# Performance work log

Measured on AMD Instinct MI355X. Metric: run time of the kernel, lower is better.

Reference implementation:

```python
import jax, jax.numpy as jnp
import numpy as np

EMB_DIM = 128
NUM_CLS = 128
H = W = 512
K = 131072


def setup_inputs() -> dict:
    key = jax.random.key(0)
    k1, k2, k3, k4 = jax.random.split(key, 4)
    gc_features = jax.random.normal(k1, (1, EMB_DIM, H, W), dtype=jnp.float32)
    cls_id_map = jax.random.randint(k2, (1, K), 0, H * W, dtype=jnp.int64)
    # nn.Linear(emb_dim, num_cls) params, kaiming-uniform-ish scale
    lim = 1.0 / np.sqrt(EMB_DIM)
    W_cls = jax.random.uniform(k3, (NUM_CLS, EMB_DIM), dtype=jnp.float32, minval=-lim, maxval=lim)
    b_cls = jax.random.uniform(k4, (NUM_CLS,), dtype=jnp.float32, minval=-lim, maxval=lim)
    return {"gc_features": gc_features, "cls_id_map": cls_id_map, "W_cls": W_cls, "b_cls": b_cls}


def reference(gc_features, cls_id_map, W_cls, b_cls):
    B, C, h, w = gc_features.shape
    # _tranpose_and_gather_feat: [B,C,H,W] -> [B,HW,C], gather rows by inds
    feat = gc_features.reshape(B, C, h * w).transpose(0, 2, 1)      # [B, HW, C]
    feat = jnp.take_along_axis(feat, cls_id_map[:, :, None], axis=1)  # [B, K, C]
    feat = feat[0]                                                   # squeeze(0) -> [K, C]
    pred = feat @ W_cls.T + b_cls                                    # [K, num_cls]
    return jax.nn.softmax(pred, axis=1)
```

## Files before the change

### kernel.cpp

```cpp
#include <hip/hip_runtime.h>
#include <hip/hip_bf16.h>
#include <hip/hip_fp16.h>

#define HW      262144
#define NCH     128
#define NCLS    128
#define KROWS   131072
#define NTILE   4096
#define CAP     192

typedef short  bf16x8 __attribute__((ext_vector_type(8)));
typedef float  f32x4  __attribute__((ext_vector_type(4)));

__device__ inline ushort f2bf(float f) {
    union { float f; unsigned u; } v; v.f = f;
    unsigned u = v.u;
    unsigned r = (u + 0x7FFFu + ((u >> 16) & 1u)) >> 16;
    return (ushort)r;
}

__global__ __launch_bounds__(256) void prep(const float* __restrict__ Wc,
                                            ushort* __restrict__ Wf,
                                            int4* __restrict__ cnt4) {
    if (blockIdx.x < 64) {
        int e    = blockIdx.x * 256 + threadIdx.x;
        int j    = e & 7;
        int slot = e >> 3;
        int lane = slot & 63;
        int kk   = (slot >> 6) & 3;
        int nt   = slot >> 8;
        int n = (nt << 4) + (lane & 15);
        int k = (kk << 5) + ((lane >> 4) << 3) + j;
        Wf[e] = f2bf(Wc[n * NCH + k]);
    } else {
        cnt4[(blockIdx.x - 64) * 256 + threadIdx.x] = make_int4(0, 0, 0, 0);
    }
}

__global__ __launch_bounds__(256) void csr_fill(const int* __restrict__ idx,
                                                int* __restrict__ cnt,
                                                int* __restrict__ pairs) {
    int k = blockIdx.x * 256 + threadIdx.x;
    int p = idx[k];
    int tile = p >> 6;
    int pos = atomicAdd(&cnt[tile], 1);
    if (pos < CAP) pairs[tile * CAP + pos] = (k << 6) | (p & 63);
}

__global__ __launch_bounds__(256) void gemm_scatter(const float* __restrict__ gc,
                                                    const ushort* __restrict__ Wf,
                                                    const float* __restrict__ bias,
                                                    const int* __restrict__ cnt,
                                                    const int* __restrict__ pairs,
                                                    float* __restrict__ out) {
    __shared__ ushort Wl[NCLS * NCH];
    __shared__ ushort AO[64 * NCH];

    const int t    = threadIdx.x;
    const int lane = t & 63;
    const int wv   = t >> 6;
    const int l15  = lane & 15;
    const int quad = lane >> 4;
    const int m0   = blockIdx.x << 6;

    float4 va[8];
    #pragma unroll
    for (int i = 0; i < 4; ++i) {
        int q  = (i << 8) + t;
        int cp = q >> 4, mq = q & 15;
        int c0 = cp << 1, m = mq << 2;
        va[2 * i]     = *(const float4*)&gc[(size_t)c0 * HW + m0 + m];
        va[2 * i + 1] = *(const float4*)&gc[(size_t)(c0 + 1) * HW + m0 + m];
    }

    #pragma unroll
    for (int i = 0; i < 8; ++i) {
        const ushort* g = Wf + (i << 11) + (t << 3);
        ushort*       l = Wl + (i << 11) + (t << 3);
        __builtin_amdgcn_global_load_lds(
            (const __attribute__((address_space(1))) unsigned*)g,
            (__attribute__((address_space(3))) unsigned*)l, 16, 0, 0);
    }

    float bcol[8];
    #pragma unroll
    for (int nt = 0; nt < 8; ++nt) bcol[nt] = bias[(nt << 4) + l15];

    #pragma unroll
    for (int i = 0; i < 4; ++i) {
        int q  = (i << 8) + t;
        int cp = q >> 4, mq = q & 15;
        int c0 = cp << 1, m = mq << 2;
        int kk = c0 >> 5, kc2 = (c0 >> 3) & 3, j = c0 & 7;
        const float* a0 = (const float*)&va[2 * i];
        const float* a1 = (const float*)&va[2 * i + 1];
        #pragma unroll
        for (int d = 0; d < 4; ++d) {
            int row  = m + d;
            int slot = ((((row >> 4) << 2) + kk) << 6) + (row & 15) + (kc2 << 4);
            slot ^= (row >> 2) & 7;
            __hip_bfloat162 pk = __float22bfloat162_rn(make_float2(a0[d], a1[d]));
            *(ushort2*)&AO[(slot << 3) + j] = *(ushort2*)&pk;
        }
    }
    __syncthreads();

    f32x4 acc[8];
    #pragma unroll
    for (int i = 0; i < 8; ++i) acc[i] = (f32x4){0.f, 0.f, 0.f, 0.f};

    #pragma unroll
    for (int kk = 0; kk < 4; ++kk) {
        int aslot = ((((wv << 2) + kk) << 6) + lane) ^ ((((wv << 4) + l15) >> 2) & 7);
        bf16x8 a = *(const bf16x8*)&AO[aslot << 3];
        #pragma unroll
        for (int nt = 0; nt < 8; ++nt) {
            bf16x8 b = *(const bf16x8*)&Wl[((((nt << 2) + kk) << 6) + lane) << 3];
            acc[nt] = __builtin_amdgcn_mfma_f32_16x16x32_bf16(a, b, acc[nt], 0, 0, 0);
        }
    }

    float inv[4];
    #pragma unroll
    for (int rr = 0; rr < 4; ++rr) {
        float s = 0.f;
        #pragma unroll
        for (int nt = 0; nt < 8; ++nt) {
            acc[nt][rr] = __expf(acc[nt][rr] + bcol[nt]);
            s += acc[nt][rr];
        }
        s += __shfl_xor(s, 1, 64);
        s += __shfl_xor(s, 2, 64);
        s += __shfl_xor(s, 4, 64);
        s += __shfl_xor(s, 8, 64);
        inv[rr] = 1.0f / s;
    }

    const int g = ((quad & 1) << 2) | (quad & 2);
    #pragma unroll
    for (int nt = 0; nt < 8; ++nt) {
        int cl = ((nt << 1) + (l15 >> 3)) ^ g;
        #pragma unroll
        for (int rr = 0; rr < 4; ++rr) {
            int row = (wv << 4) + (quad << 2) + rr;
            AO[(row << 7) + (cl << 3) + (l15 & 7)] =
                __half_as_ushort(__float2half_rn(acc[nt][rr] * inv[rr]));
        }
    }
    __syncthreads();

    const int nb = min(cnt[blockIdx.x], CAP);
    const int* pb = pairs + blockIdx.x * CAP;
    #pragma unroll 2
    for (int e = wv; e < nb; e += 4) {
        int pk  = pb[e];
        int row = pk & 63;
        int k   = pk >> 6;
        int qd  = (row >> 2) & 3;
        int gq  = ((qd & 1) << 2) | (qd & 2);
        int cl  = (lane >> 2) ^ gq;
        __half2 h = *(const __half2*)&AO[(row << 7) + (cl << 3) + ((lane << 1) & 7)];
        float2 f = __half22float2(h);
        *(float2*)&out[((size_t)k << 7) + (lane << 1)] = f;
    }
}

extern "C" void kernel_launch(void* const* d_in, const int* in_sizes, int n_in,
                              void* d_out, int out_size, void* d_ws, size_t ws_size,
                              hipStream_t stream) {
    const float* gc   = (const float*)d_in[0];
    const int*   idx  = (const int*)d_in[1];
    const float* Wc   = (const float*)d_in[2];
    const float* bias = (const float*)d_in[3];
    float* out = (float*)d_out;

    char* ws = (char*)d_ws;
    int*    cnt   = (int*)(ws);
    int*    pairs = (int*)(ws + 0x10000);
    ushort* Wf    = (ushort*)(ws + 0x400000);

    prep        <<<dim3(68),       dim3(256), 0, stream>>>(Wc, Wf, (int4*)cnt);
    csr_fill    <<<dim3(KROWS/256),dim3(256), 0, stream>>>(idx, cnt, pairs);
    gemm_scatter<<<dim3(NTILE),    dim3(256), 0, stream>>>(gc, Wf, bias, cnt, pairs, out);
}
```

Before: 236.6 us.

## Fuse prep, CSR fill and GEMM into one persistent cooperative kernel

Replaces the three kernel launches with a single persistent cooperative kernel. Each block converts W to bf16 directly into LDS, zeroes the counters, and issues its first tile's feature loads. It then passes a grid sync, builds the CSR bucket lists, syncs again, and loops over tiles while prefetching the next tile's features into registers. This removes two launch gaps and overlaps the first feature loads with the bucketing phase, at the cost of two grid-wide barriers, redundant per-block W conversion, and lower occupancy from persistent scheduling with extra registers.

```diff
diff --git a/kernel.cpp b/kernel.cpp
--- a/kernel.cpp
+++ b/kernel.cpp
@@ -1,6 +1,9 @@
 #include <hip/hip_runtime.h>
 #include <hip/hip_bf16.h>
 #include <hip/hip_fp16.h>
+#include <hip/hip_cooperative_groups.h>
+
+namespace cg = cooperative_groups;
 
 #define HW      262144
 #define NCH     128
@@ -15,44 +18,17 @@
 __device__ inline ushort f2bf(float f) {
     union { float f; unsigned u; } v; v.f = f;
     unsigned u = v.u;
-    unsigned r = (u + 0x7FFFu + ((u >> 16) & 1u)) >> 16;
-    return (ushort)r;
+    return (ushort)((u + 0x7FFFu + ((u >> 16) & 1u)) >> 16);
 }
 
-__global__ __launch_bounds__(256) void prep(const float* __restrict__ Wc,
-                                            ushort* __restrict__ Wf,
-                                            int4* __restrict__ cnt4) {
-    if (blockIdx.x < 64) {
-        int e    = blockIdx.x * 256 + threadIdx.x;
-        int j    = e & 7;
-        int slot = e >> 3;
-        int lane = slot & 63;
-        int kk   = (slot >> 6) & 3;
-        int nt   = slot >> 8;
-        int n = (nt << 4) + (lane & 15);
-        int k = (kk << 5) + ((lane >> 4) << 3) + j;
-        Wf[e] = f2bf(Wc[n * NCH + k]);
-    } else {
-        cnt4[(blockIdx.x - 64) * 256 + threadIdx.x] = make_int4(0, 0, 0, 0);
-    }
-}
-
-__global__ __launch_bounds__(256) void csr_fill(const int* __restrict__ idx,
-                                                int* __restrict__ cnt,
-                                                int* __restrict__ pairs) {
-    int k = blockIdx.x * 256 + threadIdx.x;
-    int p = idx[k];
-    int tile = p >> 6;
-    int pos = atomicAdd(&cnt[tile], 1);
-    if (pos < CAP) pairs[tile * CAP + pos] = (k << 6) | (p & 63);
-}
-
-__global__ __launch_bounds__(256) void gemm_scatter(const float* __restrict__ gc,
-                                                    const ushort* __restrict__ Wf,
-                                                    const float* __restrict__ bias,
-                                                    const int* __restrict__ cnt,
-                                                    const int* __restrict__ pairs,
-                                                    float* __restrict__ out) {
+__global__ __launch_bounds__(256, 3) void fused(
+        const float* __restrict__ gc,
+        const int*   __restrict__ idx,
+        const float* __restrict__ Wc,
+        const float* __restrict__ bias,
+        int*         __restrict__ cnt,
+        int*         __restrict__ pairs,
+        float*       __restrict__ out) {
     __shared__ ushort Wl[NCLS * NCH];
     __shared__ ushort AO[64 * NCH];
 
@@ -61,107 +37,157 @@
     const int wv   = t >> 6;
     const int l15  = lane & 15;
     const int quad = lane >> 4;
-    const int m0   = blockIdx.x << 6;
+    const int nthr = (int)gridDim.x << 8;
+    const int gtid = ((int)blockIdx.x << 8) + t;
+
+    #pragma unroll
+    for (int s = 0; s < 8; ++s) {
+        int slot = (s << 8) + t;
+        int ln = slot & 63;
+        int kk = (slot >> 6) & 3;
+        int nt = slot >> 8;
+        int n  = (nt << 4) + (ln & 15);
+        int k0 = (kk << 5) + ((ln >> 4) << 3);
+        const float* wp = Wc + n * NCH + k0;
+        float4 w0 = *(const float4*)wp;
+        float4 w1 = *(const float4*)(wp + 4);
+        ushort u[8];
+        u[0] = f2bf(w0.x); u[1] = f2bf(w0.y); u[2] = f2bf(w0.z); u[3] = f2bf(w0.w);
+        u[4] = f2bf(w1.x); u[5] = f2bf(w1.y); u[6] = f2bf(w1.z); u[7] = f2bf(w1.w);
+        *(bf16x8*)&Wl[slot << 3] = *(bf16x8*)u;
+    }
+
+    for (int i = gtid; i < NTILE; i += nthr) cnt[i] = 0;
 
     float4 va[8];
-    #pragma unroll
-    for (int i = 0; i < 4; ++i) {
-        int q  = (i << 8) + t;
-        int cp = q >> 4, mq = q & 15;
-        int c0 = cp << 1, m = mq << 2;
-        va[2 * i]     = *(const float4*)&gc[(size_t)c0 * HW + m0 + m];
-        va[2 * i + 1] = *(const float4*)&gc[(size_t)(c0 + 1) * HW + m0 + m];
-    }
-
-    #pragma unroll
-    for (int i = 0; i < 8; ++i) {
-        const ushort* g = Wf + (i << 11) + (t << 3);
-        ushort*       l = Wl + (i << 11) + (t << 3);
-        __builtin_amdgcn_global_load_lds(
-            (const __attribute__((address_space(1))) unsigned*)g,
-            (__attribute__((address_space(3))) unsigned*)l, 16, 0, 0);
-    }
+    int tt = blockIdx.x;
+    {
+        const int m0 = tt << 6;
+        #pragma unroll
+        for (int i = 0; i < 4; ++i) {
+            int q  = (i << 8) + t;
+            int cp = q >> 4, mq = q & 15;
+            int c0 = cp << 1, m = mq << 2;
+            va[2 * i]     = *(const float4*)&gc[(size_t)c0 * HW + m0 + m];
+            va[2 * i + 1] = *(const float4*)&gc[(size_t)(c0 + 1) * HW + m0 + m];
+        }
+    }
+
+    cg::this_grid().sync();
+
+    for (int k = gtid; k < KROWS; k += nthr) {
+        int p = idx[k];
+        int tile = p >> 6;
+        int pos = atomicAdd(&cnt[tile], 1);
+        if (pos < CAP) pairs[tile * CAP + pos] = (k << 6) | (p & 63);
+    }
+    __threadfence();
+
+    cg::this_grid().sync();
 
     float bcol[8];
     #pragma unroll
     for (int nt = 0; nt < 8; ++nt) bcol[nt] = bias[(nt << 4) + l15];
 
-    #pragma unroll
-    for (int i = 0; i < 4; ++i) {
-        int q  = (i << 8) + t;
-        int cp = q >> 4, mq = q & 15;
-        int c0 = cp << 1, m = mq << 2;
-        int kk = c0 >> 5, kc2 = (c0 >> 3) & 3, j = c0 & 7;
-        const float* a0 = (const float*)&va[2 * i];
-        const float* a1 = (const float*)&va[2 * i + 1];
-        #pragma unroll
-        for (int d = 0; d < 4; ++d) {
-            int row  = m + d;
-            int slot = ((((row >> 4) << 2) + kk) << 6) + (row & 15) + (kc2 << 4);
-            slot ^= (row >> 2) & 7;
-            __hip_bfloat162 pk = __float22bfloat162_rn(make_float2(a0[d], a1[d]));
-            *(ushort2*)&AO[(slot << 3) + j] = *(ushort2*)&pk;
-        }
-    }
-    __syncthreads();
-
-    f32x4 acc[8];
-    #pragma unroll
-    for (int i = 0; i < 8; ++i) acc[i] = (f32x4){0.f, 0.f, 0.f, 0.f};
-
-    #pragma unroll
-    for (int kk = 0; kk < 4; ++kk) {
-        int aslot = ((((wv << 2) + kk) << 6) + lane) ^ ((((wv << 4) + l15) >> 2) & 7);
-        bf16x8 a = *(const bf16x8*)&AO[aslot << 3];
+    const int stride = (int)gridDim.x;
+    for (; tt < NTILE; tt += stride) {
+        #pragma unroll
+        for (int i = 0; i < 4; ++i) {
+            int q  = (i << 8) + t;
+            int cp = q >> 4, mq = q & 15;
+            int c0 = cp << 1, m = mq << 2;
+            int kk = c0 >> 5, kc2 = (c0 >> 3) & 3, j = c0 & 7;
+            const float* a0 = (const float*)&va[2 * i];
+            const float* a1 = (const float*)&va[2 * i + 1];
+            #pragma unroll
+            for (int d = 0; d < 4; ++d) {
+                int row  = m + d;
+                int slot = ((((row >> 4) << 2) + kk) << 6) + (row & 15) + (kc2 << 4);
+                slot ^= (row >> 2) & 7;
+                __hip_bfloat162 pk = __float22bfloat162_rn(make_float2(a0[d], a1[d]));
+                *(ushort2*)&AO[(slot << 3) + j] = *(ushort2*)&pk;
+            }
+        }
+        __syncthreads();
+
+        const int tn = tt + stride;
+        float4 vb[8];
+        if (tn < NTILE) {
+            const int m1 = tn << 6;
+            #pragma unroll
+            for (int i = 0; i < 4; ++i) {
+                int q  = (i << 8) + t;
+                int cp = q >> 4, mq = q & 15;
+                int c0 = cp << 1, m = mq << 2;
+                vb[2 * i]     = *(const float4*)&gc[(size_t)c0 * HW + m1 + m];
+                vb[2 * i + 1] = *(const float4*)&gc[(size_t)(c0 + 1) * HW + m1 + m];
+            }
+        }
+
+        f32x4 acc[8];
+        #pragma unroll
+        for (int i = 0; i < 8; ++i) acc[i] = (f32x4){0.f, 0.f, 0.f, 0.f};
+
+        #pragma unroll
+        for (int kk = 0; kk < 4; ++kk) {
+            int aslot = ((((wv << 2) + kk) << 6) + lane) ^ ((((wv << 4) + l15) >> 2) & 7);
+            bf16x8 a = *(const bf16x8*)&AO[aslot << 3];
+            #pragma unroll
+            for (int nt = 0; nt < 8; ++nt) {
+                bf16x8 b = *(const bf16x8*)&Wl[((((nt << 2) + kk) << 6) + lane) << 3];
+                acc[nt] = __builtin_amdgcn_mfma_f32_16x16x32_bf16(a, b, acc[nt], 0, 0, 0);
+            }
+        }
+
+        float inv[4];
+        #pragma unroll
+        for (int rr = 0; rr < 4; ++rr) {
+            float s = 0.f;
+            #pragma unroll
+            for (int nt = 0; nt < 8; ++nt) {
+                acc[nt][rr] = __expf(acc[nt][rr] + bcol[nt]);
+                s += acc[nt][rr];
+            }
+            s += __shfl_xor(s, 1, 64);
+            s += __shfl_xor(s, 2, 64);
+            s += __shfl_xor(s, 4, 64);
+            s += __shfl_xor(s, 8, 64);
+            inv[rr] = 1.0f / s;
+        }
+
+        const int g = ((quad & 1) << 2) | (quad & 2);
         #pragma unroll
         for (int nt = 0; nt < 8; ++nt) {
-            bf16x8 b = *(const bf16x8*)&Wl[((((nt << 2) + kk) << 6) + lane) << 3];
-            acc[nt] = __builtin_amdgcn_mfma_f32_16x16x32_bf16(a, b, acc[nt], 0, 0, 0);
-        }
-    }
-
-    float inv[4];
-    #pragma unroll
-    for (int rr = 0; rr < 4; ++rr) {
-        float s = 0.f;
-        #pragma unroll
-        for (int nt = 0; nt < 8; ++nt) {
-            acc[nt][rr] = __expf(acc[nt][rr] + bcol[nt]);
-            s += acc[nt][rr];
-        }
-        s += __shfl_xor(s, 1, 64);
-        s += __shfl_xor(s, 2, 64);
-        s += __shfl_xor(s, 4, 64);
-        s += __shfl_xor(s, 8, 64);
-        inv[rr] = 1.0f / s;
-    }
-
-    const int g = ((quad & 1) << 2) | (quad & 2);
-    #pragma unroll
-    for (int nt = 0; nt < 8; ++nt) {
-        int cl = ((nt << 1) + (l15 >> 3)) ^ g;
-        #pragma unroll
-        for (int rr = 0; rr < 4; ++rr) {
-            int row = (wv << 4) + (quad << 2) + rr;
-            AO[(row << 7) + (cl << 3) + (l15 & 7)] =
-                __half_as_ushort(__float2half_rn(acc[nt][rr] * inv[rr]));
-        }
-    }
-    __syncthreads();
-
-    const int nb = min(cnt[blockIdx.x], CAP);
-    const int* pb = pairs + blockIdx.x * CAP;
-    #pragma unroll 2
-    for (int e = wv; e < nb; e += 4) {
-        int pk  = pb[e];
-        int row = pk & 63;
-        int k   = pk >> 6;
-        int qd  = (row >> 2) & 3;
-        int gq  = ((qd & 1) << 2) | (qd & 2);
-        int cl  = (lane >> 2) ^ gq;
-        __half2 h = *(const __half2*)&AO[(row << 7) + (cl << 3) + ((lane << 1) & 7)];
-        float2 f = __half22float2(h);
-        *(float2*)&out[((size_t)k << 7) + (lane << 1)] = f;
+            int cl = ((nt << 1) + (l15 >> 3)) ^ g;
+            #pragma unroll
+            for (int rr = 0; rr < 4; ++rr) {
+                int row = (wv << 4) + (quad << 2) + rr;
+                AO[(row << 7) + (cl << 3) + (l15 & 7)] =
+                    __half_as_ushort(__float2half_rn(acc[nt][rr] * inv[rr]));
+            }
+        }
+        __syncthreads();
+
+        const int nb = min(cnt[tt], CAP);
+        const int* pb = pairs + tt * CAP;
+        #pragma unroll 2
+        for (int e = wv; e < nb; e += 4) {
+            int pk  = pb[e];
+            int row = pk & 63;
+            int k   = pk >> 6;
+            int qd  = (row >> 2) & 3;
+            int gq  = ((qd & 1) << 2) | (qd & 2);
+            int cl  = (lane >> 2) ^ gq;
+            __half2 h = *(const __half2*)&AO[(row << 7) + (cl << 3) + ((lane << 1) & 7)];
+            float2 f = __half22float2(h);
+            *(float2*)&out[((size_t)k << 7) + (lane << 1)] = f;
+        }
+        __syncthreads();
+
+        if (tn < NTILE) {
+            #pragma unroll
+            for (int i = 0; i < 8; ++i) va[i] = vb[i];
+        }
     }
 }
 
@@ -175,11 +201,24 @@
     float* out = (float*)d_out;
 
     char* ws = (char*)d_ws;
-    int*    cnt   = (int*)(ws);
-    int*    pairs = (int*)(ws + 0x10000);
-    ushort* Wf    = (ushort*)(ws + 0x400000);
-
-    prep        <<<dim3(68),       dim3(256), 0, stream>>>(Wc, Wf, (int4*)cnt);
-    csr_fill    <<<dim3(KROWS/256),dim3(256), 0, stream>>>(idx, cnt, pairs);
-    gemm_scatter<<<dim3(NTILE),    dim3(256), 0, stream>>>(gc, Wf, bias, cnt, pairs, out);
+    int* cnt   = (int*)(ws);
+    int* pairs = (int*)(ws + 0x10000);
+
+    static int nblk = 0;
+    if (nblk == 0) {
+        int occ = 0;
+        if (hipOccupancyMaxActiveBlocksPerMultiprocessor(&occ, fused, 256, 0) != hipSuccess || occ < 1)
+            occ = 1;
+        if (occ > 16) occ = 16;
+        int ncu = 256;
+        hipDeviceProp_t prop;
+        if (hipGetDeviceProperties(&prop, 0) == hipSuccess && prop.multiProcessorCount > 0)
+            ncu = prop.multiProcessorCount;
+        nblk = occ * ncu;
+        if (nblk > NTILE) nblk = NTILE;
+    }
+
+    void* args[] = {(void*)&gc, (void*)&idx, (void*)&Wc, (void*)&bias,
+                    (void*)&cnt, (void*)&pairs, (void*)&out};
+    hipLaunchCooperativeKernel(fused, dim3(nblk), dim3(256), args, 0, stream);
 }
```

After: 355.9 us. 50.4% more time.
